# Kernel tuning notes

Measured on AMD Instinct MI355X. Metric: run time of the kernel, lower is better.

The kernel has to match this reference:

```python
import jax, jax.numpy as jnp
import numpy as np

B, P, E = 16, 1024, 768
HID, HEADS = 768, 12
DH = HID // HEADS  # 64
EPS = 1e-5


def setup_inputs() -> dict:
    key = jax.random.key(0)
    ks = jax.random.split(key, 4)
    return {
        "x": jax.random.normal(ks[0], (B, P, E), dtype=jnp.float32),
        "ln_weight": jnp.ones((P, E), dtype=jnp.float32),
        "ln_bias": jnp.zeros((P, E), dtype=jnp.float32),
        "qkv": jax.random.normal(ks[1], (E, 3 * HID), dtype=jnp.float32),
        "lin_w": jax.random.normal(ks[2], (HID, E), dtype=jnp.float32) * 0.02,
        "lin_b": jax.random.normal(ks[3], (E,), dtype=jnp.float32) * 0.02,
    }


def reference(x, ln_weight, ln_bias, qkv, lin_w, lin_b):
    # LayerNorm over the last TWO dims (patches, emb), per torch nn.LayerNorm((P, E))
    mean = jnp.mean(x, axis=(-2, -1), keepdims=True)
    var = jnp.var(x, axis=(-2, -1), keepdims=True)
    xn = (x - mean) / jnp.sqrt(var + EPS) * ln_weight + ln_bias

    # QKV projection: [B,P,E] @ [E,3*HID] -> [B,P,3*HID]
    proj = xn @ qkv
    # view(B,P,heads,-1) then permute -> [B,heads,P,3*DH]; chunk along last dim
    proj = proj.reshape(B, P, HEADS, 3 * DH).transpose(0, 2, 1, 3)
    q, k, v = proj[..., :DH], proj[..., DH:2 * DH], proj[..., 2 * DH:]

    # Softmax-free attention: (Q K^T) V
    atten = jnp.einsum("bhqd,bhkd->bhqk", q, k)  # [B,H,P,P]
    out = jnp.einsum("bhqk,bhkd->bhqd", atten, v)  # [B,H,P,DH]

    out = out.transpose(0, 2, 1, 3).reshape(B, P, HID)
    # dropout p=0.0 (eval) -> identity
    out = jax.nn.relu(out @ lin_w + lin_b)
    return out + x
```

## Files before the change

### kernel.cpp

```cpp
#include <hip/hip_runtime.h>
#include <hip/hip_bf16.h>
#include <cstdint>

#define BB   16
#define PP   1024
#define EE   768
#define HID  768
#define NH   12
#define DH   64
#define NPB  (PP * EE)
#define MROWS (BB * PP)

typedef __bf16 bf16_t;
typedef __bf16 bf16x8 __attribute__((ext_vector_type(8)));
typedef float  f32x4  __attribute__((ext_vector_type(4)));

__device__ __forceinline__ void gld16(const void* g, void* l) {
    __builtin_amdgcn_global_load_lds(
        (const __attribute__((address_space(1))) void*)(uintptr_t)g,
        (__attribute__((address_space(3))) void*)(uint32_t)(uintptr_t)l,
        16, 0, 0);
}

__global__ __launch_bounds__(256) void stats1_kernel(const float* __restrict__ x,
                                                     float* __restrict__ part) {
    int bid = blockIdx.x;
    int b = bid >> 6, s = bid & 63;
    const float4* xp = (const float4*)(x + (size_t)b * NPB + (size_t)s * 12288);
    float sum = 0.f, ss = 0.f;
#pragma unroll
    for (int i = 0; i < 12; ++i) {
        float4 v = xp[i * 256 + threadIdx.x];
        sum += v.x + v.y + v.z + v.w;
        ss  += v.x * v.x + v.y * v.y + v.z * v.z + v.w * v.w;
    }
#pragma unroll
    for (int off = 32; off > 0; off >>= 1) {
        sum += __shfl_down(sum, off, 64);
        ss  += __shfl_down(ss,  off, 64);
    }
    __shared__ float tmp[8];
    int wave = threadIdx.x >> 6, lane = threadIdx.x & 63;
    if (lane == 0) { tmp[wave * 2] = sum; tmp[wave * 2 + 1] = ss; }
    __syncthreads();
    if (threadIdx.x == 0) {
        part[bid * 2]     = tmp[0] + tmp[2] + tmp[4] + tmp[6];
        part[bid * 2 + 1] = tmp[1] + tmp[3] + tmp[5] + tmp[7];
    }
}

__global__ __launch_bounds__(64) void stats2_kernel(const float* __restrict__ part,
                                                    float* __restrict__ stats) {
    int b = blockIdx.x, l = threadIdx.x;
    float sum = part[(b * 64 + l) * 2];
    float ss  = part[(b * 64 + l) * 2 + 1];
#pragma unroll
    for (int off = 32; off > 0; off >>= 1) {
        sum += __shfl_down(sum, off, 64);
        ss  += __shfl_down(ss,  off, 64);
    }
    if (l == 0) {
        const float inv_n = 1.f / (float)NPB;
        float mean = sum * inv_n;
        float var  = ss * inv_n - mean * mean;
        stats[b * 2]     = mean;
        stats[b * 2 + 1] = rsqrtf(var + 1e-5f);
    }
}

__global__ __launch_bounds__(256) void ln_apply_kernel(const float* __restrict__ x,
                                                       const float* __restrict__ lnw,
                                                       const float* __restrict__ lnb,
                                                       const float* __restrict__ stats,
                                                       bf16_t* __restrict__ xn) {
    int i = (blockIdx.x * 256 + threadIdx.x) * 8;
    int b = i / NPB;
    int r = i - b * NPB;
    float mean = stats[b * 2], rstd = stats[b * 2 + 1];
    float4 x0 = *(const float4*)(x + i),     x1 = *(const float4*)(x + i + 4);
    float4 w0 = *(const float4*)(lnw + r),   w1 = *(const float4*)(lnw + r + 4);
    float4 c0 = *(const float4*)(lnb + r),   c1 = *(const float4*)(lnb + r + 4);
    union { bf16_t h[8]; uint4 u; } o;
    o.h[0] = (bf16_t)((x0.x - mean) * rstd * w0.x + c0.x);
    o.h[1] = (bf16_t)((x0.y - mean) * rstd * w0.y + c0.y);
    o.h[2] = (bf16_t)((x0.z - mean) * rstd * w0.z + c0.z);
    o.h[3] = (bf16_t)((x0.w - mean) * rstd * w0.w + c0.w);
    o.h[4] = (bf16_t)((x1.x - mean) * rstd * w1.x + c1.x);
    o.h[5] = (bf16_t)((x1.y - mean) * rstd * w1.y + c1.y);
    o.h[6] = (bf16_t)((x1.z - mean) * rstd * w1.z + c1.z);
    o.h[7] = (bf16_t)((x1.w - mean) * rstd * w1.w + c1.w);
    *(uint4*)(xn + i) = o.u;
}

__global__ __launch_bounds__(256) void to_bf16_T_kernel(const float* __restrict__ src,
                                                        bf16_t* __restrict__ dst,
                                                        int R, int C) {
    int idx = blockIdx.x * 256 + threadIdx.x;
    if (idx >= R * C) return;
    int c = idx / R, r = idx - c * R;
    dst[idx] = (bf16_t)src[(size_t)r * C + c];
}

template <int KDIM>
__device__ __forceinline__ void gemm_core_128(const bf16_t* __restrict__ A,
                                              const bf16_t* __restrict__ Bt,
                                              int mBase, int nBase,
                                              f32x4 acc[4][4],
                                              bf16_t* As, bf16_t* Bs) {
    const int t = threadIdx.x;
    const int lane = t & 63, wave = t >> 6;
    const int wm = wave >> 1, wn = wave & 1;
    const int m16 = lane & 15, quad = lane >> 4;

    const int r0 = t >> 2,       s0 = t & 3, g0 = (s0 - (r0 >> 1)) & 3;
    const int r1 = 64 + (t >> 2),            g1 = (s0 - (r1 >> 1)) & 3;
    const bf16_t* pa0 = A  + (size_t)(mBase + r0) * KDIM + g0 * 8;
    const bf16_t* pa1 = A  + (size_t)(mBase + r1) * KDIM + g1 * 8;
    const bf16_t* pb0 = Bt + (size_t)(nBase + r0) * KDIM + g0 * 8;
    const bf16_t* pb1 = Bt + (size_t)(nBase + r1) * KDIM + g1 * 8;
    bf16_t* la0 = As + t * 8;         bf16_t* la1 = As + (256 + t) * 8;
    bf16_t* lb0 = Bs + t * 8;         bf16_t* lb1 = Bs + (256 + t) * 8;

    const f32x4 z = {0.f, 0.f, 0.f, 0.f};
#pragma unroll
    for (int mm = 0; mm < 4; ++mm)
#pragma unroll
        for (int nn = 0; nn < 4; ++nn) acc[mm][nn] = z;

    int raOff[4], rbOff[4];
#pragma unroll
    for (int i = 0; i < 4; ++i) {
        int ra = wm * 64 + i * 16 + m16;
        raOff[i] = ra * 32 + (((quad + (ra >> 1)) & 3) * 8);
        int rb = wn * 64 + i * 16 + m16;
        rbOff[i] = rb * 32 + (((quad + (rb >> 1)) & 3) * 8);
    }

    for (int k0 = 0; k0 < KDIM; k0 += 32) {
        __syncthreads();
        gld16(pa0 + k0, la0);  gld16(pa1 + k0, la1);
        gld16(pb0 + k0, lb0);  gld16(pb1 + k0, lb1);
        __syncthreads();
        bf16x8 af[4], bfv[4];
#pragma unroll
        for (int i = 0; i < 4; ++i) {
            af[i]  = *(const bf16x8*)(As + raOff[i]);
            bfv[i] = *(const bf16x8*)(Bs + rbOff[i]);
        }
#pragma unroll
        for (int mm = 0; mm < 4; ++mm)
#pragma unroll
            for (int nn = 0; nn < 4; ++nn)
                acc[mm][nn] = __builtin_amdgcn_mfma_f32_16x16x32_bf16(
                    af[mm], bfv[nn], acc[mm][nn], 0, 0, 0);
    }
}

__global__ __launch_bounds__(256) void gemm_qkv_kernel(const bf16_t* __restrict__ xn,
                                                       const bf16_t* __restrict__ qkvT,
                                                       bf16_t* __restrict__ q,
                                                       bf16_t* __restrict__ kt,
                                                       bf16_t* __restrict__ vt) {
    __shared__ bf16_t smem[9216];
    f32x4 acc[4][4];
    const int mBase = blockIdx.y * 128, nBase = blockIdx.x * 128;
    gemm_core_128<768>(xn, qkvT, mBase, nBase, acc, smem, smem + 4096);

    const int t = threadIdx.x;
    const int lane = t & 63, wave = t >> 6;
    const int wm = wave >> 1, wn = wave & 1;
    const int m16 = lane & 15, quad = lane >> 4;
    const int b = mBase >> 10, p0 = mBase & 1023;

#pragma unroll
    for (int half = 0; half < 2; ++half) {
        const int g = blockIdx.x * 2 + half;
        const int cls = g % 3, h = g / 3;
        const size_t bh = (size_t)(b * NH + h);
        __syncthreads();
        if (cls == 0) {
            if (wn == half) {
#pragma unroll
                for (int mm = 0; mm < 4; ++mm)
#pragma unroll
                    for (int nn = 0; nn < 4; ++nn)
#pragma unroll
                        for (int i = 0; i < 4; ++i)
                            smem[(wm * 64 + mm * 16 + quad * 4 + i) * 72 + nn * 16 + m16] =
                                (bf16_t)acc[mm][nn][i];
            }
            __syncthreads();
#pragma unroll
            for (int it = 0; it < 4; ++it) {
                int slot = it * 256 + t;
                int r = slot >> 3, cc = slot & 7;
                bf16x8 val = *(const bf16x8*)(smem + r * 72 + cc * 8);
                *(bf16x8*)(q + (bh * PP + p0 + r) * DH + cc * 8) = val;
            }
        } else {
            bf16_t* dst = (cls == 1) ? kt : vt;
            if (wn == half) {
#pragma unroll
                for (int mm = 0; mm < 4; ++mm)
#pragma unroll
                    for (int nn = 0; nn < 4; ++nn) {
                        int c = nn * 16 + m16;
                        int r0 = wm * 64 + mm * 16 + quad * 4;
                        union { bf16_t hh[4]; uint2 u; } pk;
#pragma unroll
                        for (int i = 0; i < 4; ++i) pk.hh[i] = (bf16_t)acc[mm][nn][i];
                        *(uint2*)(&smem[c * 136 + r0]) = pk.u;
                    }
            }
            __syncthreads();
#pragma unroll
            for (int it = 0; it < 4; ++it) {
                int slot = it * 256 + t;
                int d = slot >> 4, pc = slot & 15;
                bf16x8 val = *(const bf16x8*)(smem + d * 136 + pc * 8);
                *(bf16x8*)(dst + (bh * DH + d) * PP + p0 + pc * 8) = val;
            }
        }
    }
}

__global__ __launch_bounds__(256) void kv_kernel(const bf16_t* __restrict__ kt,
                                                 const bf16_t* __restrict__ vt,
                                                 bf16_t* __restrict__ thi,
                                                 bf16_t* __restrict__ tlo) {
    __shared__ float red[4 * 64 * 65];
    const int bh = blockIdx.x;
    const bf16_t* Vb = vt + (size_t)bh * DH * PP;
    const bf16_t* Kb = kt + (size_t)bh * DH * PP;
    const int t = threadIdx.x;
    const int lane = t & 63, wave = t >> 6;
    const int m16 = lane & 15, quad = lane >> 4;
    const f32x4 z = {0.f, 0.f, 0.f, 0.f};
    f32x4 acc[4][4];
#pragma unroll
    for (int mm = 0; mm < 4; ++mm)
#pragma unroll
        for (int nn = 0; nn < 4; ++nn) acc[mm][nn] = z;

    for (int ks = 0; ks < 8; ++ks) {
        int kb = wave * 256 + ks * 32 + quad * 8;
        bf16x8 af[4], bfv[4];
#pragma unroll
        for (int mm = 0; mm < 4; ++mm)
            af[mm] = *(const bf16x8*)(Vb + (size_t)(mm * 16 + m16) * PP + kb);
#pragma unroll
        for (int nn = 0; nn < 4; ++nn)
            bfv[nn] = *(const bf16x8*)(Kb + (size_t)(nn * 16 + m16) * PP + kb);
#pragma unroll
        for (int mm = 0; mm < 4; ++mm)
#pragma unroll
            for (int nn = 0; nn < 4; ++nn)
                acc[mm][nn] = __builtin_amdgcn_mfma_f32_16x16x32_bf16(
                    af[mm], bfv[nn], acc[mm][nn], 0, 0, 0);
    }
#pragma unroll
    for (int mm = 0; mm < 4; ++mm)
#pragma unroll
        for (int nn = 0; nn < 4; ++nn)
#pragma unroll
            for (int i = 0; i < 4; ++i)
                red[wave * 4160 + (mm * 16 + quad * 4 + i) * 65 + nn * 16 + m16] =
                    acc[mm][nn][i];
    __syncthreads();
#pragma unroll
    for (int j = 0; j < 16; ++j) {
        int idx = j * 256 + t;
        int m = idx >> 6, n = idx & 63;
        int a = m * 65 + n;
        float s = red[a] + red[4160 + a] + red[8320 + a] + red[12480 + a];
        bf16_t hi = (bf16_t)s;
        float lo = s - (float)hi;
        thi[(size_t)bh * 4096 + idx] = hi;
        tlo[(size_t)bh * 4096 + idx] = (bf16_t)lo;
    }
}

__global__ __launch_bounds__(256) void o_kernel(const bf16_t* __restrict__ q,
                                                const bf16_t* __restrict__ thi,
                                                const bf16_t* __restrict__ tlo,
                                                bf16_t* __restrict__ o) {
    __shared__ bf16_t N[128 * 72];
    const int bh = blockIdx.y;
    const int b = bh / NH, h = bh - b * NH;
    const int p0 = blockIdx.x * 128;
    const bf16_t* Qb = q + ((size_t)bh * PP + p0) * DH;
    const bf16_t* Th = thi + (size_t)bh * 4096;
    const bf16_t* Tl = tlo + (size_t)bh * 4096;
    const int t = threadIdx.x;
    const int lane = t & 63, wave = t >> 6;
    const int m16 = lane & 15, quad = lane >> 4;
    const f32x4 z = {0.f, 0.f, 0.f, 0.f};
    f32x4 acc[2][4];
#pragma unroll
    for (int mm = 0; mm < 2; ++mm)
#pragma unroll
        for (int nn = 0; nn < 4; ++nn) acc[mm][nn] = z;

#pragma unroll
    for (int ks = 0; ks < 2; ++ks) {
        bf16x8 af[2], bh_[4], bl_[4];
#pragma unroll
        for (int mm = 0; mm < 2; ++mm)
            af[mm] = *(const bf16x8*)(
                Qb + (size_t)(wave * 32 + mm * 16 + m16) * DH + ks * 32 + quad * 8);
#pragma unroll
        for (int nn = 0; nn < 4; ++nn) {
            bh_[nn] = *(const bf16x8*)(Th + (nn * 16 + m16) * 64 + ks * 32 + quad * 8);
            bl_[nn] = *(const bf16x8*)(Tl + (nn * 16 + m16) * 64 + ks * 32 + quad * 8);
        }
#pragma unroll
        for (int mm = 0; mm < 2; ++mm)
#pragma unroll
            for (int nn = 0; nn < 4; ++nn) {
                acc[mm][nn] = __builtin_amdgcn_mfma_f32_16x16x32_bf16(
                    af[mm], bh_[nn], acc[mm][nn], 0, 0, 0);
                acc[mm][nn] = __builtin_amdgcn_mfma_f32_16x16x32_bf16(
                    af[mm], bl_[nn], acc[mm][nn], 0, 0, 0);
            }
    }
#pragma unroll
    for (int mm = 0; mm < 2; ++mm)
#pragma unroll
        for (int nn = 0; nn < 4; ++nn)
#pragma unroll
            for (int i = 0; i < 4; ++i)
                N[(wave * 32 + mm * 16 + quad * 4 + i) * 72 + nn * 16 + m16] =
                    (bf16_t)acc[mm][nn][i];
    __syncthreads();
#pragma unroll
    for (int it = 0; it < 4; ++it) {
        int slot = it * 256 + t;
        int r = slot >> 3, cc = slot & 7;
        bf16x8 val = *(const bf16x8*)(N + r * 72 + cc * 8);
        *(bf16x8*)(o + ((size_t)(b * PP + p0 + r)) * HID + h * DH + cc * 8) = val;
    }
}

__global__ __launch_bounds__(256) void gemm_out_kernel(const bf16_t* __restrict__ o,
                                                       const bf16_t* __restrict__ lwT,
                                                       const float* __restrict__ linb,
                                                       const float* __restrict__ x,
                                                       float* __restrict__ out) {
    __shared__ bf16_t smem[8192];
    f32x4 acc[4][4];
    const int mBase = blockIdx.y * 128, nBase = blockIdx.x * 128;
    gemm_core_128<768>(o, lwT, mBase, nBase, acc, smem, smem + 4096);

    const int lane = threadIdx.x & 63, wave = threadIdx.x >> 6;
    const int wm = wave >> 1, wn = wave & 1;
    const int m16 = lane & 15, quad = lane >> 4;
#pragma unroll
    for (int mm = 0; mm < 4; ++mm) {
#pragma unroll
        for (int i = 0; i < 4; ++i) {
            size_t row = mBase + wm * 64 + mm * 16 + quad * 4 + i;
#pragma unroll
            for (int nn = 0; nn < 4; ++nn) {
                int col = nBase + wn * 64 + nn * 16 + m16;
                float v = acc[mm][nn][i] + linb[col];
                v = fmaxf(v, 0.f) + x[row * EE + col];
                out[row * EE + col] = v;
            }
        }
    }
}

extern "C" void kernel_launch(void* const* d_in, const int* in_sizes, int n_in,
                              void* d_out, int out_size, void* d_ws, size_t ws_size,
                              hipStream_t stream) {
    const float* x    = (const float*)d_in[0];
    const float* lnw  = (const float*)d_in[1];
    const float* lnb  = (const float*)d_in[2];
    const float* qkvw = (const float*)d_in[3];
    const float* linw = (const float*)d_in[4];
    const float* linb = (const float*)d_in[5];
    float* out = (float*)d_out;
    char* ws = (char*)d_ws;

    float*  part  = (float*)(ws + 0);
    float*  stats = (float*)(ws + 8192);
    bf16_t* xn    = (bf16_t*)(ws + 8448);
    bf16_t* qkvT  = (bf16_t*)(ws + 25174272);
    bf16_t* lwT   = (bf16_t*)(ws + 28713216);
    bf16_t* q     = (bf16_t*)(ws + 29892864);
    bf16_t* kt    = (bf16_t*)(ws + 55058688);
    bf16_t* vt    = (bf16_t*)(ws + 80224512);
    bf16_t* thi   = qkvT;
    bf16_t* tlo   = qkvT + 192 * 4096;
    bf16_t* o     = xn;

    stats1_kernel<<<dim3(BB * 64), dim3(256), 0, stream>>>(x, part);
    stats2_kernel<<<dim3(BB), dim3(64), 0, stream>>>(part, stats);
    ln_apply_kernel<<<dim3(6144), dim3(256), 0, stream>>>(x, lnw, lnb, stats, xn);
    to_bf16_T_kernel<<<dim3(6912), dim3(256), 0, stream>>>(qkvw, qkvT, 768, 2304);
    to_bf16_T_kernel<<<dim3(2304), dim3(256), 0, stream>>>(linw, lwT, 768, 768);
    gemm_qkv_kernel<<<dim3(18, 128), dim3(256), 0, stream>>>(xn, qkvT, q, kt, vt);
    kv_kernel<<<dim3(192), dim3(256), 0, stream>>>(kt, vt, thi, tlo);
    o_kernel<<<dim3(8, 192), dim3(256), 0, stream>>>(q, thi, tlo, o);
    gemm_out_kernel<<<dim3(6, 128), dim3(256), 0, stream>>>(o, lwT, linb, x, out);
}
```

Measured before the change: 293.3 us.

## Fold K^T V into the output projection and widen the GEMM K-tile

Reassociates the softmax-free attention so each (batch, head) K^T V product is multiplied by the matching slice of the output projection weights, giving a per-batch 768x768 matrix U. The output GEMM then runs directly on Q, and the separate O = Q·(K^T V) kernel is removed. The shared GEMM core now loads a 64-wide K tile per iteration with an 8-way swizzle, which halves the barrier count but doubles LDS use. The weight transposes and the stats finalization are merged into one prep kernel to save launches. The trade-off is extra rounding, because U is stored in bf16 and no longer as a hi/lo split.

```diff
diff --git a/kernel.cpp b/kernel.cpp
--- a/kernel.cpp
+++ b/kernel.cpp
@@ -49,22 +49,41 @@
     }
 }
 
-__global__ __launch_bounds__(64) void stats2_kernel(const float* __restrict__ part,
-                                                    float* __restrict__ stats) {
-    int b = blockIdx.x, l = threadIdx.x;
-    float sum = part[(b * 64 + l) * 2];
-    float ss  = part[(b * 64 + l) * 2 + 1];
-#pragma unroll
-    for (int off = 32; off > 0; off >>= 1) {
-        sum += __shfl_down(sum, off, 64);
-        ss  += __shfl_down(ss,  off, 64);
-    }
-    if (l == 0) {
-        const float inv_n = 1.f / (float)NPB;
-        float mean = sum * inv_n;
-        float var  = ss * inv_n - mean * mean;
-        stats[b * 2]     = mean;
-        stats[b * 2 + 1] = rsqrtf(var + 1e-5f);
+__global__ __launch_bounds__(256) void prep_kernel(const float* __restrict__ qkvw,
+                                                   const float* __restrict__ linw,
+                                                   const float* __restrict__ part,
+                                                   bf16_t* __restrict__ qkvT,
+                                                   bf16_t* __restrict__ lwT,
+                                                   float* __restrict__ stats) {
+    int bid = blockIdx.x;
+    if (bid < 6912) {
+        int idx = bid * 256 + threadIdx.x;
+        int c = idx / 768, r = idx - c * 768;
+        qkvT[idx] = (bf16_t)qkvw[(size_t)r * 2304 + c];
+    } else if (bid < 9216) {
+        int idx = (bid - 6912) * 256 + threadIdx.x;
+        int c = idx / 768, r = idx - c * 768;
+        lwT[idx] = (bf16_t)linw[(size_t)r * 768 + c];
+    } else {
+        int wave = threadIdx.x >> 6, lane = threadIdx.x & 63;
+#pragma unroll
+        for (int j = 0; j < 4; ++j) {
+            int b = wave * 4 + j;
+            float sum = part[(b * 64 + lane) * 2];
+            float ss  = part[(b * 64 + lane) * 2 + 1];
+#pragma unroll
+            for (int off = 32; off > 0; off >>= 1) {
+                sum += __shfl_down(sum, off, 64);
+                ss  += __shfl_down(ss,  off, 64);
+            }
+            if (lane == 0) {
+                const float inv_n = 1.f / (float)NPB;
+                float mean = sum * inv_n;
+                float var  = ss * inv_n - mean * mean;
+                stats[b * 2]     = mean;
+                stats[b * 2 + 1] = rsqrtf(var + 1e-5f);
+            }
+        }
     }
 }
 
@@ -92,15 +111,6 @@
     *(uint4*)(xn + i) = o.u;
 }
 
-__global__ __launch_bounds__(256) void to_bf16_T_kernel(const float* __restrict__ src,
-                                                        bf16_t* __restrict__ dst,
-                                                        int R, int C) {
-    int idx = blockIdx.x * 256 + threadIdx.x;
-    if (idx >= R * C) return;
-    int c = idx / R, r = idx - c * R;
-    dst[idx] = (bf16_t)src[(size_t)r * C + c];
-}
-
 template <int KDIM>
 __device__ __forceinline__ void gemm_core_128(const bf16_t* __restrict__ A,
                                               const bf16_t* __restrict__ Bt,
@@ -112,47 +122,57 @@
     const int wm = wave >> 1, wn = wave & 1;
     const int m16 = lane & 15, quad = lane >> 4;
 
-    const int r0 = t >> 2,       s0 = t & 3, g0 = (s0 - (r0 >> 1)) & 3;
-    const int r1 = 64 + (t >> 2),            g1 = (s0 - (r1 >> 1)) & 3;
-    const bf16_t* pa0 = A  + (size_t)(mBase + r0) * KDIM + g0 * 8;
-    const bf16_t* pa1 = A  + (size_t)(mBase + r1) * KDIM + g1 * 8;
-    const bf16_t* pb0 = Bt + (size_t)(nBase + r0) * KDIM + g0 * 8;
-    const bf16_t* pb1 = Bt + (size_t)(nBase + r1) * KDIM + g1 * 8;
-    bf16_t* la0 = As + t * 8;         bf16_t* la1 = As + (256 + t) * 8;
-    bf16_t* lb0 = Bs + t * 8;         bf16_t* lb1 = Bs + (256 + t) * 8;
-
-    const f32x4 z = {0.f, 0.f, 0.f, 0.f};
-#pragma unroll
-    for (int mm = 0; mm < 4; ++mm)
-#pragma unroll
-        for (int nn = 0; nn < 4; ++nn) acc[mm][nn] = z;
-
-    int raOff[4], rbOff[4];
+    const int sr = t >> 3, s8 = t & 7;
+    const bf16_t* pa[4]; const bf16_t* pb[4];
+#pragma unroll
+    for (int i = 0; i < 4; ++i) {
+        int row = i * 32 + sr;
+        int g = (s8 - (row & 7)) & 7;
+        pa[i] = A  + (size_t)(mBase + row) * KDIM + g * 8;
+        pb[i] = Bt + (size_t)(nBase + row) * KDIM + g * 8;
+    }
+
+    int raOff[4][2], rbOff[4][2];
 #pragma unroll
     for (int i = 0; i < 4; ++i) {
         int ra = wm * 64 + i * 16 + m16;
-        raOff[i] = ra * 32 + (((quad + (ra >> 1)) & 3) * 8);
         int rb = wn * 64 + i * 16 + m16;
-        rbOff[i] = rb * 32 + (((quad + (rb >> 1)) & 3) * 8);
-    }
-
-    for (int k0 = 0; k0 < KDIM; k0 += 32) {
+#pragma unroll
+        for (int ks = 0; ks < 2; ++ks) {
+            raOff[i][ks] = ra * 64 + (((ks * 4 + quad) + (ra & 7)) & 7) * 8;
+            rbOff[i][ks] = rb * 64 + (((ks * 4 + quad) + (rb & 7)) & 7) * 8;
+        }
+    }
+
+    const f32x4 z = {0.f, 0.f, 0.f, 0.f};
+#pragma unroll
+    for (int mm = 0; mm < 4; ++mm)
+#pragma unroll
+        for (int nn = 0; nn < 4; ++nn) acc[mm][nn] = z;
+
+    for (int k0 = 0; k0 < KDIM; k0 += 64) {
         __syncthreads();
-        gld16(pa0 + k0, la0);  gld16(pa1 + k0, la1);
-        gld16(pb0 + k0, lb0);  gld16(pb1 + k0, lb1);
+#pragma unroll
+        for (int i = 0; i < 4; ++i) {
+            gld16(pa[i] + k0, As + i * 2048 + t * 8);
+            gld16(pb[i] + k0, Bs + i * 2048 + t * 8);
+        }
         __syncthreads();
-        bf16x8 af[4], bfv[4];
-#pragma unroll
-        for (int i = 0; i < 4; ++i) {
-            af[i]  = *(const bf16x8*)(As + raOff[i]);
-            bfv[i] = *(const bf16x8*)(Bs + rbOff[i]);
-        }
-#pragma unroll
-        for (int mm = 0; mm < 4; ++mm)
-#pragma unroll
-            for (int nn = 0; nn < 4; ++nn)
-                acc[mm][nn] = __builtin_amdgcn_mfma_f32_16x16x32_bf16(
-                    af[mm], bfv[nn], acc[mm][nn], 0, 0, 0);
+#pragma unroll
+        for (int ks = 0; ks < 2; ++ks) {
+            bf16x8 af[4], bfv[4];
+#pragma unroll
+            for (int i = 0; i < 4; ++i) {
+                af[i]  = *(const bf16x8*)(As + raOff[i][ks]);
+                bfv[i] = *(const bf16x8*)(Bs + rbOff[i][ks]);
+            }
+#pragma unroll
+            for (int mm = 0; mm < 4; ++mm)
+#pragma unroll
+                for (int nn = 0; nn < 4; ++nn)
+                    acc[mm][nn] = __builtin_amdgcn_mfma_f32_16x16x32_bf16(
+                        af[mm], bfv[nn], acc[mm][nn], 0, 0, 0);
+        }
     }
 }
 
@@ -161,10 +181,10 @@
                                                        bf16_t* __restrict__ q,
                                                        bf16_t* __restrict__ kt,
                                                        bf16_t* __restrict__ vt) {
-    __shared__ bf16_t smem[9216];
+    __shared__ bf16_t smem[16384];
     f32x4 acc[4][4];
     const int mBase = blockIdx.y * 128, nBase = blockIdx.x * 128;
-    gemm_core_128<768>(xn, qkvT, mBase, nBase, acc, smem, smem + 4096);
+    gemm_core_128<768>(xn, qkvT, mBase, nBase, acc, smem, smem + 8192);
 
     const int t = threadIdx.x;
     const int lane = t & 63, wave = t >> 6;
@@ -195,7 +215,7 @@
                 int slot = it * 256 + t;
                 int r = slot >> 3, cc = slot & 7;
                 bf16x8 val = *(const bf16x8*)(smem + r * 72 + cc * 8);
-                *(bf16x8*)(q + (bh * PP + p0 + r) * DH + cc * 8) = val;
+                *(bf16x8*)(q + ((size_t)(b * PP + p0 + r)) * HID + h * DH + cc * 8) = val;
             }
         } else {
             bf16_t* dst = (cls == 1) ? kt : vt;
@@ -230,8 +250,8 @@
                                                  bf16_t* __restrict__ tlo) {
     __shared__ float red[4 * 64 * 65];
     const int bh = blockIdx.x;
+    const bf16_t* Kb = kt + (size_t)bh * DH * PP;
     const bf16_t* Vb = vt + (size_t)bh * DH * PP;
-    const bf16_t* Kb = kt + (size_t)bh * DH * PP;
     const int t = threadIdx.x;
     const int lane = t & 63, wave = t >> 6;
     const int m16 = lane & 15, quad = lane >> 4;
@@ -247,10 +267,10 @@
         bf16x8 af[4], bfv[4];
 #pragma unroll
         for (int mm = 0; mm < 4; ++mm)
-            af[mm] = *(const bf16x8*)(Vb + (size_t)(mm * 16 + m16) * PP + kb);
+            af[mm] = *(const bf16x8*)(Kb + (size_t)(mm * 16 + m16) * PP + kb);
 #pragma unroll
         for (int nn = 0; nn < 4; ++nn)
-            bfv[nn] = *(const bf16x8*)(Kb + (size_t)(nn * 16 + m16) * PP + kb);
+            bfv[nn] = *(const bf16x8*)(Vb + (size_t)(nn * 16 + m16) * PP + kb);
 #pragma unroll
         for (int mm = 0; mm < 4; ++mm)
 #pragma unroll
@@ -280,76 +300,71 @@
     }
 }
 
-__global__ __launch_bounds__(256) void o_kernel(const bf16_t* __restrict__ q,
-                                                const bf16_t* __restrict__ thi,
+__global__ __launch_bounds__(256) void u_kernel(const bf16_t* __restrict__ thi,
                                                 const bf16_t* __restrict__ tlo,
-                                                bf16_t* __restrict__ o) {
-    __shared__ bf16_t N[128 * 72];
-    const int bh = blockIdx.y;
+                                                const bf16_t* __restrict__ lwT,
+                                                bf16_t* __restrict__ ut) {
+    const int bh = blockIdx.x;
     const int b = bh / NH, h = bh - b * NH;
-    const int p0 = blockIdx.x * 128;
-    const bf16_t* Qb = q + ((size_t)bh * PP + p0) * DH;
+    const int nBase = blockIdx.y * 256;
     const bf16_t* Th = thi + (size_t)bh * 4096;
     const bf16_t* Tl = tlo + (size_t)bh * 4096;
-    const int t = threadIdx.x;
-    const int lane = t & 63, wave = t >> 6;
+    const int t = threadIdx.x, lane = t & 63, wave = t >> 6;
+    const int wm = wave >> 1, wn = wave & 1;
     const int m16 = lane & 15, quad = lane >> 4;
     const f32x4 z = {0.f, 0.f, 0.f, 0.f};
-    f32x4 acc[2][4];
+    f32x4 acc[2][8];
 #pragma unroll
     for (int mm = 0; mm < 2; ++mm)
 #pragma unroll
-        for (int nn = 0; nn < 4; ++nn) acc[mm][nn] = z;
+        for (int nn = 0; nn < 8; ++nn) acc[mm][nn] = z;
 
 #pragma unroll
     for (int ks = 0; ks < 2; ++ks) {
-        bf16x8 af[2], bh_[4], bl_[4];
+        bf16x8 ah[2], al[2], bfr[8];
+#pragma unroll
+        for (int mm = 0; mm < 2; ++mm) {
+            ah[mm] = *(const bf16x8*)(Th + (wm * 32 + mm * 16 + m16) * 64 + ks * 32 + quad * 8);
+            al[mm] = *(const bf16x8*)(Tl + (wm * 32 + mm * 16 + m16) * 64 + ks * 32 + quad * 8);
+        }
+#pragma unroll
+        for (int nn = 0; nn < 8; ++nn)
+            bfr[nn] = *(const bf16x8*)(
+                lwT + (size_t)(nBase + wn * 128 + nn * 16 + m16) * 768 + h * 64 + ks * 32 + quad * 8);
 #pragma unroll
         for (int mm = 0; mm < 2; ++mm)
-            af[mm] = *(const bf16x8*)(
-                Qb + (size_t)(wave * 32 + mm * 16 + m16) * DH + ks * 32 + quad * 8);
-#pragma unroll
-        for (int nn = 0; nn < 4; ++nn) {
-            bh_[nn] = *(const bf16x8*)(Th + (nn * 16 + m16) * 64 + ks * 32 + quad * 8);
-            bl_[nn] = *(const bf16x8*)(Tl + (nn * 16 + m16) * 64 + ks * 32 + quad * 8);
-        }
-#pragma unroll
-        for (int mm = 0; mm < 2; ++mm)
-#pragma unroll
-            for (int nn = 0; nn < 4; ++nn) {
+#pragma unroll
+            for (int nn = 0; nn < 8; ++nn) {
                 acc[mm][nn] = __builtin_amdgcn_mfma_f32_16x16x32_bf16(
-                    af[mm], bh_[nn], acc[mm][nn], 0, 0, 0);
+                    ah[mm], bfr[nn], acc[mm][nn], 0, 0, 0);
                 acc[mm][nn] = __builtin_amdgcn_mfma_f32_16x16x32_bf16(
-                    af[mm], bl_[nn], acc[mm][nn], 0, 0, 0);
+                    al[mm], bfr[nn], acc[mm][nn], 0, 0, 0);
             }
     }
 #pragma unroll
     for (int mm = 0; mm < 2; ++mm)
 #pragma unroll
-        for (int nn = 0; nn < 4; ++nn)
-#pragma unroll
-            for (int i = 0; i < 4; ++i)
-                N[(wave * 32 + mm * 16 + quad * 4 + i) * 72 + nn * 16 + m16] =
-                    (bf16_t)acc[mm][nn][i];
-    __syncthreads();
-#pragma unroll
-    for (int it = 0; it < 4; ++it) {
-        int slot = it * 256 + t;
-        int r = slot >> 3, cc = slot & 7;
-        bf16x8 val = *(const bf16x8*)(N + r * 72 + cc * 8);
-        *(bf16x8*)(o + ((size_t)(b * PP + p0 + r)) * HID + h * DH + cc * 8) = val;
-    }
-}
-
-__global__ __launch_bounds__(256) void gemm_out_kernel(const bf16_t* __restrict__ o,
-                                                       const bf16_t* __restrict__ lwT,
+        for (int nn = 0; nn < 8; ++nn) {
+            int e  = nBase + wn * 128 + nn * 16 + m16;
+            int d1 = wm * 32 + mm * 16 + quad * 4;
+            union { bf16_t hh[4]; uint2 u; } pk;
+#pragma unroll
+            for (int i = 0; i < 4; ++i) pk.hh[i] = (bf16_t)acc[mm][nn][i];
+            *(uint2*)(ut + ((size_t)b * 768 + e) * 768 + h * 64 + d1) = pk.u;
+        }
+}
+
+__global__ __launch_bounds__(256) void gemm_out_kernel(const bf16_t* __restrict__ q,
+                                                       const bf16_t* __restrict__ ut,
                                                        const float* __restrict__ linb,
                                                        const float* __restrict__ x,
                                                        float* __restrict__ out) {
-    __shared__ bf16_t smem[8192];
+    __shared__ bf16_t smem[16384];
     f32x4 acc[4][4];
     const int mBase = blockIdx.y * 128, nBase = blockIdx.x * 128;
-    gemm_core_128<768>(o, lwT, mBase, nBase, acc, smem, smem + 4096);
+    const int b = mBase >> 10;
+    gemm_core_128<768>(q, ut + (size_t)b * 768 * 768, mBase, nBase, acc,
+                       smem, smem + 8192);
 
     const int lane = threadIdx.x & 63, wave = threadIdx.x >> 6;
     const int wm = wave >> 1, wn = wave & 1;
@@ -392,15 +407,13 @@
     bf16_t* vt    = (bf16_t*)(ws + 80224512);
     bf16_t* thi   = qkvT;
     bf16_t* tlo   = qkvT + 192 * 4096;
-    bf16_t* o     = xn;
+    bf16_t* ut    = kt;
 
     stats1_kernel<<<dim3(BB * 64), dim3(256), 0, stream>>>(x, part);
-    stats2_kernel<<<dim3(BB), dim3(64), 0, stream>>>(part, stats);
+    prep_kernel<<<dim3(9217), dim3(256), 0, stream>>>(qkvw, linw, part, qkvT, lwT, stats);
     ln_apply_kernel<<<dim3(6144), dim3(256), 0, stream>>>(x, lnw, lnb, stats, xn);
-    to_bf16_T_kernel<<<dim3(6912), dim3(256), 0, stream>>>(qkvw, qkvT, 768, 2304);
-    to_bf16_T_kernel<<<dim3(2304), dim3(256), 0, stream>>>(linw, lwT, 768, 768);
     gemm_qkv_kernel<<<dim3(18, 128), dim3(256), 0, stream>>>(xn, qkvT, q, kt, vt);
     kv_kernel<<<dim3(192), dim3(256), 0, stream>>>(kt, vt, thi, tlo);
-    o_kernel<<<dim3(8, 192), dim3(256), 0, stream>>>(q, thi, tlo, o);
-    gemm_out_kernel<<<dim3(6, 128), dim3(256), 0, stream>>>(o, lwT, linb, x, out);
-}
+    u_kernel<<<dim3(192, 3), dim3(256), 0, stream>>>(thi, tlo, lwT, ut);
+    gemm_out_kernel<<<dim3(6, 128), dim3(256), 0, stream>>>(q, ut, linb, x, out);
+}
```

Result: no change. 288.6 us (-1.6%).
